# Kernel optimization log

Hardware: AMD Instinct MI355X
Metric: run time of the kernel (lower is better)

Reference implementation:

```python
import jax, jax.numpy as jnp
import numpy as np

EMBED_DIM = 1024
NUM_HEADS = 16
HEAD_DIM = EMBED_DIM // NUM_HEADS
WINDOW = 128


def setup_inputs() -> dict:
    key = jax.random.key(0)
    ks = jax.random.split(key, 9)
    B, T, C = 1, 2048, EMBED_DIM
    s = 1.0 / np.sqrt(C)
    inp = {
        "x": jax.random.normal(ks[0], (B, T, C), dtype=jnp.float32),
        "wq": jax.random.normal(ks[1], (C, C), dtype=jnp.float32) * s,
        "bq": jnp.zeros((C,), dtype=jnp.float32),
        "wk": jax.random.normal(ks[2], (C, C), dtype=jnp.float32) * s,
        "bk": jnp.zeros((C,), dtype=jnp.float32),
        "wv": jax.random.normal(ks[3], (C, C), dtype=jnp.float32) * s,
        "bv": jnp.zeros((C,), dtype=jnp.float32),
        "wo": jax.random.normal(ks[4], (C, C), dtype=jnp.float32) * s,
        "bo": jnp.zeros((C,), dtype=jnp.float32),
    }
    return inp


def reference(x, wq, bq, wk, bk, wv, bv, wo, bo):
    B, T, C = x.shape
    H, D, W = NUM_HEADS, HEAD_DIM, WINDOW

    def proj(w, b):
        # torch Linear: y = x @ w.T + b ; -> (B, H, T, D)
        return (x @ w.T + b).reshape(B, T, H, D).transpose(0, 2, 1, 3)

    q = proj(wq, bq)
    k = proj(wk, bk)
    v = proj(wv, bv)

    # window index map: position t attends to keys [t-W+1, t]; zero-padded before 0
    idx = jnp.arange(T)[:, None] + jnp.arange(W)[None, :] - (W - 1)  # (T, W)
    valid = (idx >= 0)
    idxc = jnp.clip(idx, 0, T - 1)

    kw = k[:, :, idxc]                                 # (B, H, T, W, D)
    vw = v[:, :, idxc] * valid[None, None, :, :, None]  # zero padded values

    # zero-key padding gives raw score exactly 0 (inside the softmax)
    scores = jnp.einsum('bhtd,bhtwd->bhtw', q, kw)
    scores = jnp.where(valid[None, None], scores, 0.0) / np.sqrt(D)
    attn = jax.nn.softmax(scores, axis=-1)             # (B, H, T, W)

    ctx = jnp.einsum('bhtw,bhtwd->bhtd', attn, vw)     # (B, H, T, D)
    out = ctx.transpose(0, 2, 1, 3).reshape(B, T, C)
    return out @ wo.T + bo
```

## Files before the change

kernel.cpp:

```cpp
#include <hip/hip_runtime.h>


#define TSEQ 2048
#define CDIM 1024
#define HNUM 16
#define DHEAD 64
#define WWIN 128

typedef __attribute__((ext_vector_type(8))) short bf16x8;
typedef __attribute__((ext_vector_type(4))) float f32x4;

__device__ __forceinline__ unsigned short f2bf(float f) {
  unsigned u = __float_as_uint(f);
  u = (u + 0x7fffu + ((u >> 16) & 1u)) >> 16;
  return (unsigned short)u;
}
__device__ __forceinline__ float bf2f(unsigned short s) {
  return __uint_as_float(((unsigned)s) << 16);
}

__device__ __forceinline__ void gload16(const void* g, void* l) {
  __builtin_amdgcn_global_load_lds(
      (const __attribute__((address_space(1))) unsigned int*)g,
      (__attribute__((address_space(3))) unsigned int*)l, 16, 0, 0);
}

__global__ void split_bf16(const float* s0, const float* s1, const float* s2,
                           const float* s3,
                           unsigned short* h0, unsigned short* h1,
                           unsigned short* h2, unsigned short* h3,
                           unsigned short* l0, unsigned short* l1,
                           unsigned short* l2, unsigned short* l3, int n4) {
  const int z = blockIdx.z;
  const float* __restrict__ src = z == 0 ? s0 : (z == 1 ? s1 : (z == 2 ? s2 : s3));
  unsigned short* __restrict__ h = z == 0 ? h0 : (z == 1 ? h1 : (z == 2 ? h2 : h3));
  unsigned short* __restrict__ l = z == 0 ? l0 : (z == 1 ? l1 : (z == 2 ? l2 : l3));
  const int i = blockIdx.x * 256 + threadIdx.x;
  if (i >= n4) return;
  const float4 v = ((const float4*)src)[i];
  ushort4 hh, ll;
  hh.x = f2bf(v.x); ll.x = f2bf(v.x - bf2f(hh.x));
  hh.y = f2bf(v.y); ll.y = f2bf(v.y - bf2f(hh.y));
  hh.z = f2bf(v.z); ll.z = f2bf(v.z - bf2f(hh.z));
  hh.w = f2bf(v.w); ll.w = f2bf(v.w - bf2f(hh.w));
  ((ushort4*)h)[i] = hh;
  ((ushort4*)l)[i] = ll;
}

template <int BN>
__launch_bounds__(256, 2)
__global__ void gemm_mfma_split(const unsigned short* __restrict__ Ah,
                                const unsigned short* __restrict__ Al,
                                const unsigned short* Bh0, const unsigned short* Bh1,
                                const unsigned short* Bh2,
                                const unsigned short* Bl0, const unsigned short* Bl1,
                                const unsigned short* Bl2,
                                const float* bias0, const float* bias1, const float* bias2,
                                float* C0, float* C1, float* C2,
                                int M, int N, int K) {
  constexpr int NJ = BN / 32;
  constexpr int QB = BN / 64;
  const int z = blockIdx.z;
  const unsigned short* __restrict__ Bh = z == 0 ? Bh0 : (z == 1 ? Bh1 : Bh2);
  const unsigned short* __restrict__ Bl = z == 0 ? Bl0 : (z == 1 ? Bl1 : Bl2);
  const float* __restrict__ bias = z == 0 ? bias0 : (z == 1 ? bias1 : bias2);
  float* __restrict__ C = z == 0 ? C0 : (z == 1 ? C1 : C2);

  __shared__ unsigned short lAh[64 * 32], lAl[64 * 32];
  __shared__ unsigned short lBh[BN * 32], lBl[BN * 32];

  const int tid = threadIdx.x;
  const int w = tid >> 6, lane = tid & 63;
  const int wr = w >> 1, wc = w & 1;
  const int bm = blockIdx.y * 64, bn = blockIdx.x * BN;

  const int sA = tid;
  const int rA = sA >> 2;
  const int cA = ((sA & 3) ^ ((rA >> 1) & 3)) * 8;
  const int oA = (w * 64) * 8;
  int srowB[QB], scolB[QB], soffB[QB];
#pragma unroll
  for (int q = 0; q < QB; ++q) {
    const int s = w * 64 * QB + q * 64 + lane;
    const int r = s >> 2;
    srowB[q] = r;
    scolB[q] = ((s & 3) ^ ((r >> 1) & 3)) * 8;
    soffB[q] = (w * 64 * QB + q * 64) * 8;
  }
  int aoff[2], boff[NJ];
#pragma unroll
  for (int i = 0; i < 2; ++i) {
    const int ra = wr * 32 + i * 16 + (lane & 15);
    aoff[i] = ra * 32 + (((lane >> 4) ^ ((ra >> 1) & 3)) * 8);
  }
#pragma unroll
  for (int j = 0; j < NJ; ++j) {
    const int rb = wc * (BN / 2) + j * 16 + (lane & 15);
    boff[j] = rb * 32 + (((lane >> 4) ^ ((rb >> 1) & 3)) * 8);
  }

  f32x4 acc[2][NJ];
#pragma unroll
  for (int i = 0; i < 2; ++i)
#pragma unroll
    for (int j = 0; j < NJ; ++j) acc[i][j] = {0.f, 0.f, 0.f, 0.f};

  const unsigned short* gAh = Ah + (size_t)bm * K;
  const unsigned short* gAl = Al + (size_t)bm * K;
  const unsigned short* gBh = Bh + (size_t)bn * K;
  const unsigned short* gBl = Bl + (size_t)bn * K;

  for (int k0 = 0; k0 < K; k0 += 32) {
    {
      const size_t goA = (size_t)rA * K + k0 + cA;
      gload16(gAh + goA, &lAh[oA]);
      gload16(gAl + goA, &lAl[oA]);
    }
#pragma unroll
    for (int q = 0; q < QB; ++q) {
      const size_t go = (size_t)srowB[q] * K + k0 + scolB[q];
      gload16(gBh + go, &lBh[soffB[q]]);
      gload16(gBl + go, &lBl[soffB[q]]);
    }
    __syncthreads();

    bf16x8 fah[2], fal[2], fbh[NJ], fbl[NJ];
#pragma unroll
    for (int i = 0; i < 2; ++i) {
      fah[i] = *(const bf16x8*)&lAh[aoff[i]];
      fal[i] = *(const bf16x8*)&lAl[aoff[i]];
    }
#pragma unroll
    for (int j = 0; j < NJ; ++j) {
      fbh[j] = *(const bf16x8*)&lBh[boff[j]];
      fbl[j] = *(const bf16x8*)&lBl[boff[j]];
    }
#pragma unroll
    for (int i = 0; i < 2; ++i)
#pragma unroll
      for (int j = 0; j < NJ; ++j) {
        acc[i][j] = __builtin_amdgcn_mfma_f32_16x16x32_bf16(fah[i], fbh[j], acc[i][j], 0, 0, 0);
        acc[i][j] = __builtin_amdgcn_mfma_f32_16x16x32_bf16(fah[i], fbl[j], acc[i][j], 0, 0, 0);
        acc[i][j] = __builtin_amdgcn_mfma_f32_16x16x32_bf16(fal[i], fbh[j], acc[i][j], 0, 0, 0);
      }
    __syncthreads();
  }

  const int colb = bn + wc * (BN / 2) + (lane & 15);
  const int rowb = bm + wr * 32 + ((lane >> 4) << 2);
#pragma unroll
  for (int j = 0; j < NJ; ++j) {
    const int col = colb + j * 16;
    const float bv = bias[col];
#pragma unroll
    for (int i = 0; i < 2; ++i) {
      const int row = rowb + i * 16;
#pragma unroll
      for (int r = 0; r < 4; ++r)
        C[(size_t)(row + r) * N + col] = acc[i][j][r] + bv;
    }
  }
}

__launch_bounds__(256, 2)
__global__ void gemm_bt(const float* __restrict__ A,
                        const float* __restrict__ Bw0, const float* __restrict__ Bw1,
                        const float* __restrict__ Bw2,
                        const float* __restrict__ bias0, const float* __restrict__ bias1,
                        const float* __restrict__ bias2,
                        float* __restrict__ C0, float* __restrict__ C1, float* __restrict__ C2,
                        int M, int N, int K) {
  const int z = blockIdx.z;
  const float* __restrict__ B = (z == 0) ? Bw0 : ((z == 1) ? Bw1 : Bw2);
  const float* __restrict__ bias = (z == 0) ? bias0 : ((z == 1) ? bias1 : bias2);
  float* __restrict__ C = (z == 0) ? C0 : ((z == 1) ? C1 : C2);

  __shared__ float As[16][132];
  __shared__ float Bs[16][132];

  const int tid = threadIdx.x;
  const int tx = tid & 15;
  const int ty = tid >> 4;
  const int bm = blockIdx.y * 128;
  const int bn = blockIdx.x * 128;
  const int lrow = tid >> 2;
  const int lk = (tid & 3) << 2;

  float acc[8][8] = {};

  for (int k0 = 0; k0 < K; k0 += 16) {
#pragma unroll
    for (int r = 0; r < 2; ++r) {
      const int row = (r << 6) + lrow;
      const float4 a4 = *(const float4*)(A + (size_t)(bm + row) * K + k0 + lk);
      As[lk + 0][row] = a4.x; As[lk + 1][row] = a4.y;
      As[lk + 2][row] = a4.z; As[lk + 3][row] = a4.w;
      const float4 b4 = *(const float4*)(B + (size_t)(bn + row) * K + k0 + lk);
      Bs[lk + 0][row] = b4.x; Bs[lk + 1][row] = b4.y;
      Bs[lk + 2][row] = b4.z; Bs[lk + 3][row] = b4.w;
    }
    __syncthreads();
#pragma unroll
    for (int k = 0; k < 16; ++k) {
      float a[8], b[8];
      *(float4*)(a)     = *(const float4*)(&As[k][ty * 8]);
      *(float4*)(a + 4) = *(const float4*)(&As[k][ty * 8 + 4]);
      *(float4*)(b)     = *(const float4*)(&Bs[k][tx * 8]);
      *(float4*)(b + 4) = *(const float4*)(&Bs[k][tx * 8 + 4]);
#pragma unroll
      for (int i = 0; i < 8; ++i)
#pragma unroll
        for (int j = 0; j < 8; ++j)
          acc[i][j] = fmaf(a[i], b[j], acc[i][j]);
    }
    __syncthreads();
  }

#pragma unroll
  for (int i = 0; i < 8; ++i) {
    const int row = bm + ty * 8 + i;
#pragma unroll
    for (int j4 = 0; j4 < 2; ++j4) {
      const int col = bn + tx * 8 + j4 * 4;
      const float4 bb = *(const float4*)(bias + col);
      float4 o;
      o.x = acc[i][j4 * 4 + 0] + bb.x;
      o.y = acc[i][j4 * 4 + 1] + bb.y;
      o.z = acc[i][j4 * 4 + 2] + bb.z;
      o.w = acc[i][j4 * 4 + 3] + bb.w;
      *(float4*)(C + (size_t)row * N + col) = o;
    }
  }
}

__launch_bounds__(512)
__global__ void swa_attn(const float* __restrict__ Q, const float* __restrict__ K,
                         const float* __restrict__ V, float* __restrict__ Of,
                         unsigned short* __restrict__ Oh, unsigned short* __restrict__ Ol,
                         int pack) {
  __shared__ float kb[160 * 64];
  __shared__ float qs[32 * 64];
  __shared__ float ps[8 * 4 * 132];

  const int h = blockIdx.y;
  const int t0 = blockIdx.x * 32;
  const int tid = threadIdx.x;
  const int hoff = h * DHEAD;

  for (int i = tid; i < 160 * 16; i += 512) {
    const int x = i >> 4;
    const int cp = i & 15;
    const int c = cp ^ (x & 15);
    const int key = t0 - (WWIN - 1) + x;
    float4 kv = make_float4(0.f, 0.f, 0.f, 0.f);
    if (key >= 0 && key < TSEQ)
      kv = *(const float4*)(K + (size_t)key * CDIM + hoff + 4 * c);
    *(float4*)&kb[x * 64 + 4 * cp] = kv;
  }
  for (int i = tid; i < 32 * 16; i += 512) {
    const int xq = i >> 4;
    const int c = i & 15;
    *(float4*)&qs[xq * 64 + 4 * c] =
        *(const float4*)(Q + (size_t)(t0 + xq) * CDIM + hoff + 4 * c);
  }
  for (int i = tid; i < 8 * 4 * 132; i += 512) ps[i] = 0.f;
  __syncthreads();

  const int w = tid >> 6;
  const int L = tid & 63;
  const int q0 = w * 4;

  const int x0 = q0 + L;
  const int xm = x0 & 15;
  const float* kp0 = kb + x0 * 64;
  const float* kp1 = kp0 + 64 * 64;
  const int x2 = (x0 + 128 < 160) ? (x0 + 128) : 159;
  const float* kp2 = kb + x2 * 64;
  const float* qp = qs + q0 * 64;

  float s0[4] = {0.f, 0.f, 0.f, 0.f};
  float s1[4] = {0.f, 0.f, 0.f, 0.f};
  float s2[4] = {0.f, 0.f, 0.f, 0.f};
#pragma unroll
  for (int dc = 0; dc < 16; ++dc) {
    const int co = 4 * (dc ^ xm);
    const float4 k0 = *(const float4*)(kp0 + co);
    const float4 k1 = *(const float4*)(kp1 + co);
    const float4 k2 = *(const float4*)(kp2 + co);
#pragma unroll
    for (int q = 0; q < 4; ++q) {
      const float4 qv = *(const float4*)(qp + q * 64 + 4 * dc);
      s0[q] = fmaf(qv.x, k0.x, fmaf(qv.y, k0.y, fmaf(qv.z, k0.z, fmaf(qv.w, k0.w, s0[q]))));
      s1[q] = fmaf(qv.x, k1.x, fmaf(qv.y, k1.y, fmaf(qv.z, k1.z, fmaf(qv.w, k1.w, s1[q]))));
      if (q > 0)
        s2[q] = fmaf(qv.x, k2.x, fmaf(qv.y, k2.y, fmaf(qv.z, k2.z, fmaf(qv.w, k2.w, s2[q]))));
    }
  }

  float inv[4];
#pragma unroll
  for (int q = 0; q < 4; ++q) {
    const bool lo = (L >= q);
    const float sa = (lo ? s0[q] : s2[q]) * 0.125f;
    const float sb = s1[q] * 0.125f;

    float m = fmaxf(sa, sb);
#pragma unroll
    for (int off = 32; off > 0; off >>= 1) m = fmaxf(m, __shfl_xor(m, off));
    const float pa = __expf(sa - m);
    const float pb = __expf(sb - m);
    float sum = pa + pb;
#pragma unroll
    for (int off = 32; off > 0; off >>= 1) sum += __shfl_xor(sum, off);
    inv[q] = 1.0f / sum;

    float* psq = ps + (w * 4 + q) * 132;
    psq[lo ? L : (128 + L)] = pa;
    psq[64 + L] = pb;
  }

  float accq[4] = {0.f, 0.f, 0.f, 0.f};
  const float* psb = ps + w * 4 * 132;
#pragma unroll 4
  for (int ci = 0; ci < 33; ++ci) {
    const int xr = 4 * ci;
    const float4 pq0 = *(const float4*)(psb + 0 * 132 + xr);
    const float4 pq1 = *(const float4*)(psb + 1 * 132 + xr);
    const float4 pq2 = *(const float4*)(psb + 2 * 132 + xr);
    const float4 pq3 = *(const float4*)(psb + 3 * 132 + xr);
#pragma unroll
    for (int xi = 0; xi < 4; ++xi) {
      const int x = q0 + xr + xi;
      const int key = t0 - (WWIN - 1) + x;
      float vx = 0.f;
      if (key >= 0) {
        const int kc = key < TSEQ ? key : TSEQ - 1;
        vx = V[(size_t)kc * CDIM + hoff + L];
      }
      const float f0 = (xi == 0) ? pq0.x : (xi == 1) ? pq0.y : (xi == 2) ? pq0.z : pq0.w;
      const float f1 = (xi == 0) ? pq1.x : (xi == 1) ? pq1.y : (xi == 2) ? pq1.z : pq1.w;
      const float f2 = (xi == 0) ? pq2.x : (xi == 1) ? pq2.y : (xi == 2) ? pq2.z : pq2.w;
      const float f3 = (xi == 0) ? pq3.x : (xi == 1) ? pq3.y : (xi == 2) ? pq3.z : pq3.w;
      accq[0] = fmaf(f0, vx, accq[0]);
      accq[1] = fmaf(f1, vx, accq[1]);
      accq[2] = fmaf(f2, vx, accq[2]);
      accq[3] = fmaf(f3, vx, accq[3]);
    }
  }

#pragma unroll
  for (int q = 0; q < 4; ++q) {
    const size_t idx = (size_t)(t0 + q0 + q) * CDIM + hoff + L;
    const float o = accq[q] * inv[q];
    if (pack) {
      const unsigned short hv = f2bf(o);
      Oh[idx] = hv;
      Ol[idx] = f2bf(o - bf2f(hv));
    } else {
      Of[idx] = o;
    }
  }
}

extern "C" void kernel_launch(void* const* d_in, const int* in_sizes, int n_in,
                              void* d_out, int out_size, void* d_ws, size_t ws_size,
                              hipStream_t stream) {
  const float* x  = (const float*)d_in[0];
  const float* wq = (const float*)d_in[1];
  const float* bq = (const float*)d_in[2];
  const float* wk = (const float*)d_in[3];
  const float* bk = (const float*)d_in[4];
  const float* wv = (const float*)d_in[5];
  const float* bv = (const float*)d_in[6];
  const float* wo = (const float*)d_in[7];
  const float* bo = (const float*)d_in[8];
  float* out = (float*)d_out;

  const size_t MB = 1024 * 1024;
  const size_t NTOK = (size_t)TSEQ * CDIM;

  if (ws_size >= 48 * MB) {
    char* wsb = (char*)d_ws;
    unsigned short* Whq = (unsigned short*)(wsb + 0 * MB);
    unsigned short* Wlq = (unsigned short*)(wsb + 2 * MB);
    unsigned short* Whk = (unsigned short*)(wsb + 4 * MB);
    unsigned short* Wlk = (unsigned short*)(wsb + 6 * MB);
    unsigned short* Whv = (unsigned short*)(wsb + 8 * MB);
    unsigned short* Wlv = (unsigned short*)(wsb + 10 * MB);
    unsigned short* Who = (unsigned short*)(wsb + 12 * MB);
    unsigned short* Wlo = (unsigned short*)(wsb + 14 * MB);
    float* Qw = (float*)(wsb + 16 * MB);
    float* Kw = (float*)(wsb + 24 * MB);
    float* Vw = (float*)(wsb + 32 * MB);
    unsigned short* Ch = (unsigned short*)(wsb + 40 * MB);
    unsigned short* Cl = (unsigned short*)(wsb + 44 * MB);
    unsigned short* Xh = (unsigned short*)d_out;
    unsigned short* Xl = Xh + NTOK;

    {
      dim3 gx((int)(NTOK / 4 / 256), 1, 1);
      split_bf16<<<gx, 256, 0, stream>>>(x, x, x, x, Xh, Xh, Xh, Xh,
                                         Xl, Xl, Xl, Xl, (int)(NTOK / 4));
      const int wn4 = CDIM * CDIM / 4;
      dim3 gw(wn4 / 256, 1, 4);
      split_bf16<<<gw, 256, 0, stream>>>(wq, wk, wv, wo, Whq, Whk, Whv, Who,
                                         Wlq, Wlk, Wlv, Wlo, wn4);
    }

    dim3 gqkv(CDIM / 128, TSEQ / 64, 3);
    gemm_mfma_split<128><<<gqkv, 256, 0, stream>>>(Xh, Xl, Whq, Whk, Whv,
                                                   Wlq, Wlk, Wlv,
                                                   bq, bk, bv, Qw, Kw, Vw,
                                                   TSEQ, CDIM, CDIM);

    dim3 gattn(TSEQ / 32, HNUM);
    swa_attn<<<gattn, 512, 0, stream>>>(Qw, Kw, Vw, (float*)0, Ch, Cl, 1);

    dim3 gout(CDIM / 64, TSEQ / 64, 1);
    gemm_mfma_split<64><<<gout, 256, 0, stream>>>(Ch, Cl, Who, Who, Who,
                                                  Wlo, Wlo, Wlo,
                                                  bo, bo, bo, out, out, out,
                                                  TSEQ, CDIM, CDIM);
  } else {
    float* Qw = (float*)d_ws;
    float* Kw = Qw + NTOK;
    float* Vw = Kw + NTOK;
    float* Cw = Vw + NTOK;

    dim3 gqkv(CDIM / 128, TSEQ / 128, 3);
    gemm_bt<<<gqkv, 256, 0, stream>>>(x, wq, wk, wv, bq, bk, bv, Qw, Kw, Vw,
                                      TSEQ, CDIM, CDIM);

    dim3 gattn(TSEQ / 32, HNUM);
    swa_attn<<<gattn, 512, 0, stream>>>(Qw, Kw, Vw, Cw, (unsigned short*)0,
                                        (unsigned short*)0, 0);

    dim3 gout(CDIM / 128, TSEQ / 128, 1);
    gemm_bt<<<gout, 256, 0, stream>>>(Cw, wo, wo, wo, bo, bo, bo, out, out, out,
                                      TSEQ, CDIM, CDIM);
  }
}
```

Baseline: 202.2 us.

## Double-buffer LDS tiles in split-bf16 GEMM and swizzle attention block order

The split-bf16 MFMA GEMM now uses two LDS buffers. The next K-tile's global-to-LDS loads are issued before the current tile's MFMAs, and one barrier per iteration is removed, so load latency can overlap with compute. The attention kernel changes from a 2D grid to a 1D grid of 1024 blocks with an XCD-style swizzle, so that neighbouring time blocks of the same head land on the same chiplet and share the overlapping K/V window in L2. In exchange, the GEMM's LDS use doubles, which may lower occupancy under launch_bounds(256,2).

```diff
diff --git a/kernel.cpp b/kernel.cpp
--- a/kernel.cpp
+++ b/kernel.cpp
@@ -60,14 +60,16 @@
                                 int M, int N, int K) {
   constexpr int NJ = BN / 32;
   constexpr int QB = BN / 64;
+  constexpr int ASZ = 64 * 32;
+  constexpr int BSZ = BN * 32;
   const int z = blockIdx.z;
   const unsigned short* __restrict__ Bh = z == 0 ? Bh0 : (z == 1 ? Bh1 : Bh2);
   const unsigned short* __restrict__ Bl = z == 0 ? Bl0 : (z == 1 ? Bl1 : Bl2);
   const float* __restrict__ bias = z == 0 ? bias0 : (z == 1 ? bias1 : bias2);
   float* __restrict__ C = z == 0 ? C0 : (z == 1 ? C1 : C2);
 
-  __shared__ unsigned short lAh[64 * 32], lAl[64 * 32];
-  __shared__ unsigned short lBh[BN * 32], lBl[BN * 32];
+  __shared__ unsigned short lAh[2 * ASZ], lAl[2 * ASZ];
+  __shared__ unsigned short lBh[2 * BSZ], lBl[2 * BSZ];
 
   const int tid = threadIdx.x;
   const int w = tid >> 6, lane = tid & 63;
@@ -110,30 +112,37 @@
   const unsigned short* gBh = Bh + (size_t)bn * K;
   const unsigned short* gBl = Bl + (size_t)bn * K;
 
-  for (int k0 = 0; k0 < K; k0 += 32) {
-    {
-      const size_t goA = (size_t)rA * K + k0 + cA;
-      gload16(gAh + goA, &lAh[oA]);
-      gload16(gAl + goA, &lAl[oA]);
-    }
+  auto STAGE = [&](int buf, int k0) {
+    const int ab = buf * ASZ, bb = buf * BSZ;
+    const size_t goA = (size_t)rA * K + k0 + cA;
+    gload16(gAh + goA, &lAh[ab + oA]);
+    gload16(gAl + goA, &lAl[ab + oA]);
 #pragma unroll
     for (int q = 0; q < QB; ++q) {
       const size_t go = (size_t)srowB[q] * K + k0 + scolB[q];
-      gload16(gBh + go, &lBh[soffB[q]]);
-      gload16(gBl + go, &lBl[soffB[q]]);
-    }
-    __syncthreads();
-
+      gload16(gBh + go, &lBh[bb + soffB[q]]);
+      gload16(gBl + go, &lBl[bb + soffB[q]]);
+    }
+  };
+
+  const int NT = K / 32;
+  STAGE(0, 0);
+  __syncthreads();
+  int cur = 0;
+  for (int t = 0; t < NT; ++t) {
+    if (t + 1 < NT) STAGE(cur ^ 1, (t + 1) * 32);
+
+    const int ab = cur * ASZ, bb = cur * BSZ;
     bf16x8 fah[2], fal[2], fbh[NJ], fbl[NJ];
 #pragma unroll
     for (int i = 0; i < 2; ++i) {
-      fah[i] = *(const bf16x8*)&lAh[aoff[i]];
-      fal[i] = *(const bf16x8*)&lAl[aoff[i]];
+      fah[i] = *(const bf16x8*)&lAh[ab + aoff[i]];
+      fal[i] = *(const bf16x8*)&lAl[ab + aoff[i]];
     }
 #pragma unroll
     for (int j = 0; j < NJ; ++j) {
-      fbh[j] = *(const bf16x8*)&lBh[boff[j]];
-      fbl[j] = *(const bf16x8*)&lBl[boff[j]];
+      fbh[j] = *(const bf16x8*)&lBh[bb + boff[j]];
+      fbl[j] = *(const bf16x8*)&lBl[bb + boff[j]];
     }
 #pragma unroll
     for (int i = 0; i < 2; ++i)
@@ -144,6 +153,7 @@
         acc[i][j] = __builtin_amdgcn_mfma_f32_16x16x32_bf16(fal[i], fbh[j], acc[i][j], 0, 0, 0);
       }
     __syncthreads();
+    cur ^= 1;
   }
 
   const int colb = bn + wc * (BN / 2) + (lane & 15);
@@ -242,8 +252,10 @@
   __shared__ float qs[32 * 64];
   __shared__ float ps[8 * 4 * 132];
 
-  const int h = blockIdx.y;
-  const int t0 = blockIdx.x * 32;
+  const int bid = blockIdx.x;
+  const int swz = (bid & 7) * 128 + (bid >> 3);
+  const int h = swz >> 6;
+  const int t0 = (swz & 63) * 32;
   const int tid = threadIdx.x;
   const int hoff = h * DHEAD;
 
@@ -413,8 +425,7 @@
                                                    bq, bk, bv, Qw, Kw, Vw,
                                                    TSEQ, CDIM, CDIM);
 
-    dim3 gattn(TSEQ / 32, HNUM);
-    swa_attn<<<gattn, 512, 0, stream>>>(Qw, Kw, Vw, (float*)0, Ch, Cl, 1);
+    swa_attn<<<dim3(1024), 512, 0, stream>>>(Qw, Kw, Vw, (float*)0, Ch, Cl, 1);
 
     dim3 gout(CDIM / 64, TSEQ / 64, 1);
     gemm_mfma_split<64><<<gout, 256, 0, stream>>>(Ch, Cl, Who, Who, Who,
@@ -431,9 +442,8 @@
     gemm_bt<<<gqkv, 256, 0, stream>>>(x, wq, wk, wv, bq, bk, bv, Qw, Kw, Vw,
                                       TSEQ, CDIM, CDIM);
 
-    dim3 gattn(TSEQ / 32, HNUM);
-    swa_attn<<<gattn, 512, 0, stream>>>(Qw, Kw, Vw, Cw, (unsigned short*)0,
-                                        (unsigned short*)0, 0);
+    swa_attn<<<dim3(1024), 512, 0, stream>>>(Qw, Kw, Vw, Cw, (unsigned short*)0,
+                                             (unsigned short*)0, 0);
 
     dim3 gout(CDIM / 128, TSEQ / 128, 1);
     gemm_bt<<<gout, 256, 0, stream>>>(Cw, wo, wo, wo, bo, bo, bo, out, out, out,
```

Measured after the change: 200.8 us. Within noise of the previous version (-0.7%).
